# Performance work log

Measured on AMD Instinct MI355X. Metric: run time of the kernel, lower is better.

## Reference

```python
import jax, jax.numpy as jnp
import numpy as np

N_NODES = 100000
N_EDGES = 1250000
IN_CH = 64
OUT_CH = 64


def setup_inputs() -> dict:
    key = jax.random.key(0)
    k1, k2, k3 = jax.random.split(key, 3)
    x = jax.random.normal(k1, (N_NODES, IN_CH), dtype=jnp.float32)
    edge_index = jax.random.randint(k2, (2, N_EDGES), 0, N_NODES, dtype=jnp.int64)
    # torch.nn.Linear(3*IN_CH, OUT_CH): W [out, in], b [out]
    scale = 1.0 / np.sqrt(3 * IN_CH)
    W = jax.random.uniform(k3, (OUT_CH, 3 * IN_CH), dtype=jnp.float32,
                           minval=-scale, maxval=scale)
    b = jnp.zeros((OUT_CH,), dtype=jnp.float32)
    return {"x": x, "edge_index": edge_index, "W": W, "b": b}


def reference(x, edge_index, W, b):
    src, dst = edge_index[0], edge_index[1]
    msgs = x[src]  # [E, D] gather of source node features

    agg_sum = jax.ops.segment_sum(msgs, dst, num_segments=N_NODES)  # [N, D]
    count = jax.ops.segment_sum(jnp.ones((msgs.shape[0],), dtype=x.dtype),
                                dst, num_segments=N_NODES)  # [N]
    agg_mean = agg_sum / jnp.maximum(count, 1.0)[:, None]

    agg_max = jax.ops.segment_max(msgs, dst, num_segments=N_NODES)  # [N, D]
    has_edge = (count > 0)[:, None]
    agg_max = jnp.where(has_edge, agg_max, 0.0)  # empty segments -> 0 (PyG default)

    feats = jnp.concatenate([agg_sum, agg_mean, agg_max], axis=-1)  # [N, 3D]
    return jnp.einsum('nf,of->no', feats, W) + b
```

## Files before the change

### kernel.cpp

```cpp
#include <hip/hip_runtime.h>
#include <hip/hip_bf16.h>
#include <math.h>

#define D    64
#define F3   192
#define NPB  256
#define LBITS 8
#define SBITS 17
#define NBLK 256
#define SCAN_CHUNK 2048

using bf16x8 = __attribute__((ext_vector_type(8))) short;
using f32x4  = __attribute__((ext_vector_type(4))) float;


__global__ __launch_bounds__(256) void k_bin_hist(
    const int* __restrict__ dstv, unsigned* __restrict__ bcntT,
    int E, int EPB, int NB)
{
    __shared__ unsigned h[512];
    for (int i = threadIdx.x; i < NB; i += 256) h[i] = 0;
    __syncthreads();
    int lo = blockIdx.x * EPB, hi = min(E, lo + EPB);
    for (int e = lo + threadIdx.x; e < hi; e += 256)
        atomicAdd(&h[((unsigned)dstv[e]) >> LBITS], 1u);
    __syncthreads();
    for (int i = threadIdx.x; i < NB; i += 256)
        bcntT[(size_t)i * NBLK + blockIdx.x] = h[i];
}

__global__ __launch_bounds__(256) void k_chunk_scan(
    const unsigned* __restrict__ cnt, unsigned* __restrict__ offs,
    unsigned* __restrict__ partials, int N)
{
    __shared__ unsigned ts[256];
    int t = threadIdx.x;
    int ebase = blockIdx.x * SCAN_CHUNK + t * 8;
    unsigned v[8];
    unsigned s = 0;
    #pragma unroll
    for (int j = 0; j < 8; ++j) {
        unsigned c = (ebase + j < N) ? cnt[ebase + j] : 0u;
        v[j] = s; s += c;
    }
    ts[t] = s;
    __syncthreads();
    #pragma unroll
    for (int off = 1; off < 256; off <<= 1) {
        unsigned add = (t >= off) ? ts[t - off] : 0u;
        __syncthreads();
        ts[t] += add;
        __syncthreads();
    }
    unsigned tb = (t > 0) ? ts[t - 1] : 0u;
    #pragma unroll
    for (int j = 0; j < 8; ++j)
        if (ebase + j < N) offs[ebase + j] = tb + v[j];
    if (t == 255) partials[blockIdx.x] = ts[255];
}

__global__ void k_scan_partials(unsigned* partials, int n)
{
    if (blockIdx.x == 0 && threadIdx.x == 0) {
        unsigned s = 0;
        for (int i = 0; i < n; ++i) { unsigned c = partials[i]; partials[i] = s; s += c; }
    }
}

__global__ __launch_bounds__(256) void k_add_base(
    unsigned* __restrict__ offs, const unsigned* __restrict__ partials, int N)
{
    int i = blockIdx.x * 256 + threadIdx.x;
    if (i < N) offs[i] += partials[i / SCAN_CHUNK];
}

__global__ __launch_bounds__(256) void k_bin_scatter(
    const int* __restrict__ srcv, const int* __restrict__ dstv,
    const unsigned* __restrict__ bbaseT, unsigned* __restrict__ binned,
    int E, int EPB, int NB)
{
    __shared__ unsigned cur[512];
    for (int i = threadIdx.x; i < NB; i += 256)
        cur[i] = bbaseT[(size_t)i * NBLK + blockIdx.x];
    __syncthreads();
    int lo = blockIdx.x * EPB, hi = min(E, lo + EPB);
    for (int e = lo + threadIdx.x; e < hi; e += 256) {
        unsigned d = (unsigned)dstv[e];
        unsigned s = (unsigned)srcv[e];
        unsigned p = atomicAdd(&cur[d >> LBITS], 1u);
        binned[p] = ((d & (NPB - 1u)) << SBITS) | s;
    }
}

__global__ __launch_bounds__(256) void k_bucket_csr(
    const unsigned* __restrict__ binned, const unsigned* __restrict__ bbaseT,
    unsigned* __restrict__ offs, unsigned* __restrict__ cnt,
    unsigned* __restrict__ ssrc, int E, int NB, int N)
{
    __shared__ unsigned c[256];
    __shared__ unsigned ts[256];
    int k = blockIdx.x;
    int t = threadIdx.x;
    unsigned bstart = bbaseT[(size_t)k * NBLK];
    unsigned bend   = (k + 1 < NB) ? bbaseT[(size_t)(k + 1) * NBLK] : (unsigned)E;

    c[t] = 0;
    __syncthreads();
    for (unsigned e = bstart + t; e < bend; e += 256)
        atomicAdd(&c[binned[e] >> SBITS], 1u);
    __syncthreads();

    unsigned myc = c[t];
    ts[t] = myc;
    __syncthreads();
    #pragma unroll
    for (int off = 1; off < 256; off <<= 1) {
        unsigned add = (t >= off) ? ts[t - off] : 0u;
        __syncthreads();
        ts[t] += add;
        __syncthreads();
    }
    unsigned excl = t ? ts[t - 1] : 0u;

    int gn = k * NPB + t;
    if (gn < N) { offs[gn] = bstart + excl; cnt[gn] = myc; }

    c[t] = excl;
    __syncthreads();
    for (unsigned e = bstart + t; e < bend; e += 256) {
        unsigned u  = binned[e];
        unsigned ld = u >> SBITS;
        unsigned r  = atomicAdd(&c[ld], 1u);
        ssrc[bstart + r] = u & ((1u << SBITS) - 1u);
    }
}


__device__ __forceinline__ ushort f2bf(float f) {
    __hip_bfloat16 h = __float2bfloat16(f);
    return *reinterpret_cast<ushort*>(&h);
}

__global__ __launch_bounds__(256) void k_gather(
    const float*    __restrict__ x,
    const unsigned* __restrict__ ssrc,
    const unsigned* __restrict__ offs,
    const unsigned* __restrict__ cnt,
    ushort*         __restrict__ feats,
    int N)
{
    int tid  = threadIdx.x;
    int lane = tid & 63;
    int wv   = tid >> 6;
    int g    = lane >> 4;
    int c4   = (lane & 15) << 2;

    int n = blockIdx.x * 4 + wv;
    if (n >= N) return;

    unsigned st = offs[n];
    unsigned dg = cnt[n];

    float4 sv = make_float4(0.f, 0.f, 0.f, 0.f);
    float4 mv = make_float4(-INFINITY, -INFINITY, -INFINITY, -INFINITY);

    for (unsigned i = (unsigned)g; i < dg; i += 4) {
        unsigned s = ssrc[st + i];
        float4 v = *reinterpret_cast<const float4*>(x + (size_t)s * D + c4);
        sv.x += v.x; sv.y += v.y; sv.z += v.z; sv.w += v.w;
        mv.x = fmaxf(mv.x, v.x); mv.y = fmaxf(mv.y, v.y);
        mv.z = fmaxf(mv.z, v.z); mv.w = fmaxf(mv.w, v.w);
    }

    #pragma unroll
    for (int off = 16; off <= 32; off <<= 1) {
        sv.x += __shfl_xor(sv.x, off); sv.y += __shfl_xor(sv.y, off);
        sv.z += __shfl_xor(sv.z, off); sv.w += __shfl_xor(sv.w, off);
        mv.x = fmaxf(mv.x, __shfl_xor(mv.x, off));
        mv.y = fmaxf(mv.y, __shfl_xor(mv.y, off));
        mv.z = fmaxf(mv.z, __shfl_xor(mv.z, off));
        mv.w = fmaxf(mv.w, __shfl_xor(mv.w, off));
    }

    float inv = dg ? 1.0f / (float)dg : 0.0f;
    size_t rb = (size_t)n * F3;
    if (g == 0) {
        ushort4 u = { f2bf(sv.x), f2bf(sv.y), f2bf(sv.z), f2bf(sv.w) };
        *reinterpret_cast<ushort4*>(feats + rb + c4) = u;
    } else if (g == 1) {
        ushort4 u = { f2bf(sv.x * inv), f2bf(sv.y * inv),
                      f2bf(sv.z * inv), f2bf(sv.w * inv) };
        *reinterpret_cast<ushort4*>(feats + rb + D + c4) = u;
    } else if (g == 2) {
        float4 m = mv;
        if (dg == 0) m = make_float4(0.f, 0.f, 0.f, 0.f);
        ushort4 u = { f2bf(m.x), f2bf(m.y), f2bf(m.z), f2bf(m.w) };
        *reinterpret_cast<ushort4*>(feats + rb + 2 * D + c4) = u;
    }
}

__global__ __launch_bounds__(256) void k_mlp_mfma(
    const ushort* __restrict__ feats,
    const float*  __restrict__ W,
    const float*  __restrict__ bias,
    float*        __restrict__ out,
    int N)
{
    int tid  = threadIdx.x;
    int lane = tid & 63;
    int c    = tid >> 6;
    int l16  = lane & 15;
    int kb   = (lane >> 4) << 3;

    int col = (c << 4) + l16;
    const float* wrow = W + (size_t)col * F3;

    bf16x8 bfr[6];
    #pragma unroll
    for (int ks = 0; ks < 6; ++ks) {
        float4 lo = *reinterpret_cast<const float4*>(wrow + ks * 32 + kb);
        float4 hi = *reinterpret_cast<const float4*>(wrow + ks * 32 + kb + 4);
        bf16x8 bb;
        bb[0] = (short)f2bf(lo.x); bb[1] = (short)f2bf(lo.y);
        bb[2] = (short)f2bf(lo.z); bb[3] = (short)f2bf(lo.w);
        bb[4] = (short)f2bf(hi.x); bb[5] = (short)f2bf(hi.y);
        bb[6] = (short)f2bf(hi.z); bb[7] = (short)f2bf(hi.w);
        bfr[ks] = bb;
    }
    float bo = bias[col];

    int ntiles = N >> 4;
    for (int t = blockIdx.x; t < ntiles; t += gridDim.x) {
        int n0 = t << 4;
        const ushort* arow = feats + (size_t)(n0 + l16) * F3 + kb;
        bf16x8 afr[6];
        #pragma unroll
        for (int ks = 0; ks < 6; ++ks)
            afr[ks] = *reinterpret_cast<const bf16x8*>(arow + ks * 32);

        f32x4 acc = { bo, bo, bo, bo };
        #pragma unroll
        for (int ks = 0; ks < 6; ++ks)
            acc = __builtin_amdgcn_mfma_f32_16x16x32_bf16(afr[ks], bfr[ks], acc, 0, 0, 0);

        int rbase = n0 + ((lane >> 4) << 2);
        #pragma unroll
        for (int r = 0; r < 4; ++r)
            out[(size_t)(rbase + r) * D + col] = acc[r];
    }
}

extern "C" void kernel_launch(void* const* d_in, const int* in_sizes, int n_in,
                              void* d_out, int out_size, void* d_ws, size_t ws_size,
                              hipStream_t stream)
{
    const float* x  = (const float*)d_in[0];
    const int*   ei = (const int*)d_in[1];
    const float* W  = (const float*)d_in[2];
    const float* b  = (const float*)d_in[3];
    float* out = (float*)d_out;

    int N = in_sizes[0] / D;
    int E = in_sizes[1] / 2;
    const int* srcv = ei;
    const int* dstv = ei + E;

    int NB  = (N + NPB - 1) / NPB;
    int EPB = (E + NBLK - 1) / NBLK;
    int M   = NB * NBLK;

    unsigned* bcntT    = (unsigned*)d_ws;
    unsigned* bbaseT   = bcntT + M;
    unsigned* partials = bbaseT + M;
    unsigned* offs     = partials + 64;
    unsigned* cnt      = offs + N;
    unsigned* ssrc     = cnt + N;
    unsigned* binned   = ssrc + E;
    ushort*   feats    = (ushort*)(binned + E);

    int nChunksM = (M + SCAN_CHUNK - 1) / SCAN_CHUNK;

    k_bin_hist<<<NBLK, 256, 0, stream>>>(dstv, bcntT, E, EPB, NB);
    k_chunk_scan<<<nChunksM, 256, 0, stream>>>(bcntT, bbaseT, partials, M);
    k_scan_partials<<<1, 64, 0, stream>>>(partials, nChunksM);
    k_add_base<<<(M + 255) / 256, 256, 0, stream>>>(bbaseT, partials, M);
    k_bin_scatter<<<NBLK, 256, 0, stream>>>(srcv, dstv, bbaseT, binned, E, EPB, NB);
    k_bucket_csr<<<NB, 256, 0, stream>>>(binned, bbaseT, offs, cnt, ssrc, E, NB, N);

    k_gather<<<(N + 3) / 4, 256, 0, stream>>>(x, ssrc, offs, cnt, feats, N);
    k_mlp_mfma<<<1024, 256, 0, stream>>>(feats, W, b, out, N);
}
```

Baseline: 133.4 us.

## Fuse neighbor gather with MFMA linear layer and gather bf16 node features

Merges the gather/aggregate kernel and the MFMA matmul into one persistent kernel. Each 16-node tile's sum/mean/max features are built in shared memory and fed straight to MFMA, so the bf16 feature matrix is never written to or read back from global memory. Node features are first cast to bf16 by a separate pass to halve gather traffic. Edge source indices are loaded once per wave and broadcast with shuffles, with two edges processed per step. The costs are an extra full pass over x for the cast, bf16 rounding of inputs before summation (less accurate), and two block barriers per tile.

Measured after the change: 135.9 us. Within noise of the previous version (+1.8%).

```diff
diff --git a/kernel.cpp b/kernel.cpp
--- a/kernel.cpp
+++ b/kernel.cpp
@@ -9,9 +9,36 @@
 #define SBITS 17
 #define NBLK 256
 #define SCAN_CHUNK 2048
+#define FPAD 200
 
 using bf16x8 = __attribute__((ext_vector_type(8))) short;
 using f32x4  = __attribute__((ext_vector_type(4))) float;
+
+__device__ __forceinline__ ushort f2bf(float f) {
+    __hip_bfloat16 h = __float2bfloat16(f);
+    return *reinterpret_cast<ushort*>(&h);
+}
+__device__ __forceinline__ float bf2f(ushort u) {
+    unsigned v = ((unsigned)u) << 16;
+    return __uint_as_float(v);
+}
+
+
+__global__ __launch_bounds__(256) void k_wcast(
+    const float* __restrict__ W, ushort* __restrict__ Wb, int n)
+{
+    for (int i = threadIdx.x; i < n; i += 256) Wb[i] = f2bf(W[i]);
+}
+
+__global__ __launch_bounds__(256) void k_xcast(
+    const float* __restrict__ x, ushort* __restrict__ xb, int n4)
+{
+    int i = blockIdx.x * 256 + threadIdx.x;
+    if (i >= n4) return;
+    float4 v = *reinterpret_cast<const float4*>(x + (size_t)i * 4);
+    ushort4 u = { f2bf(v.x), f2bf(v.y), f2bf(v.z), f2bf(v.w) };
+    *reinterpret_cast<ushort4*>(xb + (size_t)i * 4) = u;
+}
 
 
 __global__ __launch_bounds__(256) void k_bin_hist(
@@ -135,108 +162,113 @@
     }
 }
 
-
-__device__ __forceinline__ ushort f2bf(float f) {
-    __hip_bfloat16 h = __float2bfloat16(f);
-    return *reinterpret_cast<ushort*>(&h);
-}
-
-__global__ __launch_bounds__(256) void k_gather(
-    const float*    __restrict__ x,
+__global__ __launch_bounds__(256) void k_fused(
+    const ushort*   __restrict__ xb,
     const unsigned* __restrict__ ssrc,
     const unsigned* __restrict__ offs,
     const unsigned* __restrict__ cnt,
-    ushort*         __restrict__ feats,
+    const ushort*   __restrict__ Wb,
+    const float*    __restrict__ bias,
+    float*          __restrict__ out,
     int N)
 {
+    __shared__ ushort fl[16][FPAD];
+
     int tid  = threadIdx.x;
     int lane = tid & 63;
     int wv   = tid >> 6;
     int g    = lane >> 4;
     int c4   = (lane & 15) << 2;
-
-    int n = blockIdx.x * 4 + wv;
-    if (n >= N) return;
-
-    unsigned st = offs[n];
-    unsigned dg = cnt[n];
-
-    float4 sv = make_float4(0.f, 0.f, 0.f, 0.f);
-    float4 mv = make_float4(-INFINITY, -INFINITY, -INFINITY, -INFINITY);
-
-    for (unsigned i = (unsigned)g; i < dg; i += 4) {
-        unsigned s = ssrc[st + i];
-        float4 v = *reinterpret_cast<const float4*>(x + (size_t)s * D + c4);
-        sv.x += v.x; sv.y += v.y; sv.z += v.z; sv.w += v.w;
-        mv.x = fmaxf(mv.x, v.x); mv.y = fmaxf(mv.y, v.y);
-        mv.z = fmaxf(mv.z, v.z); mv.w = fmaxf(mv.w, v.w);
-    }
-
-    #pragma unroll
-    for (int off = 16; off <= 32; off <<= 1) {
-        sv.x += __shfl_xor(sv.x, off); sv.y += __shfl_xor(sv.y, off);
-        sv.z += __shfl_xor(sv.z, off); sv.w += __shfl_xor(sv.w, off);
-        mv.x = fmaxf(mv.x, __shfl_xor(mv.x, off));
-        mv.y = fmaxf(mv.y, __shfl_xor(mv.y, off));
-        mv.z = fmaxf(mv.z, __shfl_xor(mv.z, off));
-        mv.w = fmaxf(mv.w, __shfl_xor(mv.w, off));
-    }
-
-    float inv = dg ? 1.0f / (float)dg : 0.0f;
-    size_t rb = (size_t)n * F3;
-    if (g == 0) {
-        ushort4 u = { f2bf(sv.x), f2bf(sv.y), f2bf(sv.z), f2bf(sv.w) };
-        *reinterpret_cast<ushort4*>(feats + rb + c4) = u;
-    } else if (g == 1) {
-        ushort4 u = { f2bf(sv.x * inv), f2bf(sv.y * inv),
-                      f2bf(sv.z * inv), f2bf(sv.w * inv) };
-        *reinterpret_cast<ushort4*>(feats + rb + D + c4) = u;
-    } else if (g == 2) {
-        float4 m = mv;
-        if (dg == 0) m = make_float4(0.f, 0.f, 0.f, 0.f);
-        ushort4 u = { f2bf(m.x), f2bf(m.y), f2bf(m.z), f2bf(m.w) };
-        *reinterpret_cast<ushort4*>(feats + rb + 2 * D + c4) = u;
-    }
-}
-
-__global__ __launch_bounds__(256) void k_mlp_mfma(
-    const ushort* __restrict__ feats,
-    const float*  __restrict__ W,
-    const float*  __restrict__ bias,
-    float*        __restrict__ out,
-    int N)
-{
-    int tid  = threadIdx.x;
-    int lane = tid & 63;
-    int c    = tid >> 6;
     int l16  = lane & 15;
     int kb   = (lane >> 4) << 3;
 
-    int col = (c << 4) + l16;
-    const float* wrow = W + (size_t)col * F3;
-
+    int col = (wv << 4) + l16;
+    const ushort* wp = Wb + (size_t)col * F3 + kb;
     bf16x8 bfr[6];
     #pragma unroll
-    for (int ks = 0; ks < 6; ++ks) {
-        float4 lo = *reinterpret_cast<const float4*>(wrow + ks * 32 + kb);
-        float4 hi = *reinterpret_cast<const float4*>(wrow + ks * 32 + kb + 4);
-        bf16x8 bb;
-        bb[0] = (short)f2bf(lo.x); bb[1] = (short)f2bf(lo.y);
-        bb[2] = (short)f2bf(lo.z); bb[3] = (short)f2bf(lo.w);
-        bb[4] = (short)f2bf(hi.x); bb[5] = (short)f2bf(hi.y);
-        bb[6] = (short)f2bf(hi.z); bb[7] = (short)f2bf(hi.w);
-        bfr[ks] = bb;
-    }
+    for (int ks = 0; ks < 6; ++ks)
+        bfr[ks] = *reinterpret_cast<const bf16x8*>(wp + ks * 32);
     float bo = bias[col];
 
     int ntiles = N >> 4;
     for (int t = blockIdx.x; t < ntiles; t += gridDim.x) {
         int n0 = t << 4;
-        const ushort* arow = feats + (size_t)(n0 + l16) * F3 + kb;
+
+        #pragma unroll 1
+        for (int q = 0; q < 4; ++q) {
+            int nd = (wv << 2) + q;
+            int n  = n0 + nd;
+            unsigned st = offs[n];
+            unsigned dg = cnt[n];
+
+            float4 sv = make_float4(0.f, 0.f, 0.f, 0.f);
+            float4 mv = make_float4(-INFINITY, -INFINITY, -INFINITY, -INFINITY);
+
+            for (unsigned base = 0; base < dg; base += 64) {
+                unsigned m = min(64u, dg - base);
+                unsigned slist = ((unsigned)lane < m) ? ssrc[st + base + lane] : 0u;
+                unsigned i = 0;
+                for (; i + 8 <= m; i += 8) {
+                    unsigned s0 = (unsigned)__shfl((int)slist, (int)(i + g));
+                    unsigned s1 = (unsigned)__shfl((int)slist, (int)(i + 4 + g));
+                    ushort4 u0 = *reinterpret_cast<const ushort4*>(xb + (size_t)s0 * D + c4);
+                    ushort4 u1 = *reinterpret_cast<const ushort4*>(xb + (size_t)s1 * D + c4);
+                    float a0 = bf2f(u0.x), a1 = bf2f(u0.y), a2 = bf2f(u0.z), a3 = bf2f(u0.w);
+                    float b0 = bf2f(u1.x), b1 = bf2f(u1.y), b2 = bf2f(u1.z), b3 = bf2f(u1.w);
+                    sv.x += a0 + b0; sv.y += a1 + b1; sv.z += a2 + b2; sv.w += a3 + b3;
+                    mv.x = fmaxf(mv.x, fmaxf(a0, b0)); mv.y = fmaxf(mv.y, fmaxf(a1, b1));
+                    mv.z = fmaxf(mv.z, fmaxf(a2, b2)); mv.w = fmaxf(mv.w, fmaxf(a3, b3));
+                }
+                if (i + 4 <= m) {
+                    unsigned s0 = (unsigned)__shfl((int)slist, (int)(i + g));
+                    ushort4 u0 = *reinterpret_cast<const ushort4*>(xb + (size_t)s0 * D + c4);
+                    float a0 = bf2f(u0.x), a1 = bf2f(u0.y), a2 = bf2f(u0.z), a3 = bf2f(u0.w);
+                    sv.x += a0; sv.y += a1; sv.z += a2; sv.w += a3;
+                    mv.x = fmaxf(mv.x, a0); mv.y = fmaxf(mv.y, a1);
+                    mv.z = fmaxf(mv.z, a2); mv.w = fmaxf(mv.w, a3);
+                    i += 4;
+                }
+                if (i + (unsigned)g < m) {
+                    unsigned s0 = ssrc[st + base + i + (unsigned)g];
+                    ushort4 u0 = *reinterpret_cast<const ushort4*>(xb + (size_t)s0 * D + c4);
+                    float a0 = bf2f(u0.x), a1 = bf2f(u0.y), a2 = bf2f(u0.z), a3 = bf2f(u0.w);
+                    sv.x += a0; sv.y += a1; sv.z += a2; sv.w += a3;
+                    mv.x = fmaxf(mv.x, a0); mv.y = fmaxf(mv.y, a1);
+                    mv.z = fmaxf(mv.z, a2); mv.w = fmaxf(mv.w, a3);
+                }
+            }
+
+            #pragma unroll
+            for (int off = 16; off <= 32; off <<= 1) {
+                sv.x += __shfl_xor(sv.x, off); sv.y += __shfl_xor(sv.y, off);
+                sv.z += __shfl_xor(sv.z, off); sv.w += __shfl_xor(sv.w, off);
+                mv.x = fmaxf(mv.x, __shfl_xor(mv.x, off));
+                mv.y = fmaxf(mv.y, __shfl_xor(mv.y, off));
+                mv.z = fmaxf(mv.z, __shfl_xor(mv.z, off));
+                mv.w = fmaxf(mv.w, __shfl_xor(mv.w, off));
+            }
+
+            float inv = dg ? 1.0f / (float)dg : 0.0f;
+            if (g == 0) {
+                ushort4 u = { f2bf(sv.x), f2bf(sv.y), f2bf(sv.z), f2bf(sv.w) };
+                *reinterpret_cast<ushort4*>(&fl[nd][c4]) = u;
+            } else if (g == 1) {
+                ushort4 u = { f2bf(sv.x * inv), f2bf(sv.y * inv),
+                              f2bf(sv.z * inv), f2bf(sv.w * inv) };
+                *reinterpret_cast<ushort4*>(&fl[nd][D + c4]) = u;
+            } else if (g == 2) {
+                float4 m4 = mv;
+                if (dg == 0) m4 = make_float4(0.f, 0.f, 0.f, 0.f);
+                ushort4 u = { f2bf(m4.x), f2bf(m4.y), f2bf(m4.z), f2bf(m4.w) };
+                *reinterpret_cast<ushort4*>(&fl[nd][2 * D + c4]) = u;
+            }
+        }
+        __syncthreads();
+
         bf16x8 afr[6];
         #pragma unroll
         for (int ks = 0; ks < 6; ++ks)
-            afr[ks] = *reinterpret_cast<const bf16x8*>(arow + ks * 32);
+            afr[ks] = *reinterpret_cast<const bf16x8*>(&fl[l16][kb + ks * 32]);
 
         f32x4 acc = { bo, bo, bo, bo };
         #pragma unroll
@@ -247,6 +279,7 @@
         #pragma unroll
         for (int r = 0; r < 4; ++r)
             out[(size_t)(rbase + r) * D + col] = acc[r];
+        __syncthreads();
     }
 }
 
@@ -276,9 +309,13 @@
     unsigned* cnt      = offs + N;
     unsigned* ssrc     = cnt + N;
     unsigned* binned   = ssrc + E;
-    ushort*   feats    = (ushort*)(binned + E);
+    ushort*   xb       = (ushort*)(binned + E);
+    ushort*   Wb       = xb + (size_t)N * D;
 
     int nChunksM = (M + SCAN_CHUNK - 1) / SCAN_CHUNK;
+
+    k_wcast<<<1, 256, 0, stream>>>(W, Wb, D * F3);
+    k_xcast<<<(N * D / 4 + 255) / 256, 256, 0, stream>>>(x, xb, N * D / 4);
 
     k_bin_hist<<<NBLK, 256, 0, stream>>>(dstv, bcntT, E, EPB, NB);
     k_chunk_scan<<<nChunksM, 256, 0, stream>>>(bcntT, bbaseT, partials, M);
@@ -287,6 +324,5 @@
     k_bin_scatter<<<NBLK, 256, 0, stream>>>(srcv, dstv, bbaseT, binned, E, EPB, NB);
     k_bucket_csr<<<NB, 256, 0, stream>>>(binned, bbaseT, offs, cnt, ssrc, E, NB, N);
 
-    k_gather<<<(N + 3) / 4, 256, 0, stream>>>(x, ssrc, offs, cnt, feats, N);
-    k_mlp_mfma<<<1024, 256, 0, stream>>>(feats, W, b, out, N);
-}
+    k_fused<<<2048, 256, 0, stream>>>(xb, ssrc, offs, cnt, Wb, b, out, N);
+}
```
